# Kernel tuning notes

Measured on AMD Instinct MI355X. Metric: run time of the kernel, lower is better.

## Reference

```python
import jax, jax.numpy as jnp
import numpy as np

HUGE = 1e9  # stand-in for ops.HUGE_INT


def setup_inputs() -> dict:
    key = jax.random.key(0)
    ks = jax.random.split(key, 8)
    B, Q, K = 8, 128, 256
    Dq = Dk = Dv = H = 512
    query = jax.random.normal(ks[0], (B, Q, Dq), dtype=jnp.float32)
    k_ = jax.random.normal(ks[1], (B, K, Dk), dtype=jnp.float32)
    value = jax.random.normal(ks[2], (B, K, Dv), dtype=jnp.float32)
    mask = jax.random.randint(ks[3], (B, K), 0, 2, dtype=jnp.int32)
    # FFN params: linear1 (Dq+Dk -> H, bias), linear2 (H -> 1, no bias)
    W1 = jax.random.normal(ks[4], (Dq + Dk, H), dtype=jnp.float32) * 0.05
    b1 = jax.random.normal(ks[5], (H,), dtype=jnp.float32) * 0.05
    w2 = jax.random.normal(ks[6], (H, 1), dtype=jnp.float32) * 0.05
    return {"query": query, "key": k_, "value": value, "mask": mask,
            "W1": W1, "b1": b1, "w2": w2}


def reference(query, key, value, mask, W1, b1, w2):
    # Additive (FFN) attention. Original tiles query/key into [B, Q*K, Dq+Dk]
    # and applies linear1; concat@W1 is separable, so we project q and k
    # separately and broadcast-add (same math, no tiled concat tensor).
    Dq = query.shape[-1]
    Wq, Wk = W1[:Dq], W1[Dq:]
    q_proj = jnp.einsum('bqd,dh->bqh', query, Wq)   # [B,Q,H]
    k_proj = jnp.einsum('bkd,dh->bkh', key, Wk)     # [B,K,H]
    hidden = jnp.tanh(q_proj[:, :, None, :] + k_proj[:, None, :, :] + b1)  # [B,Q,K,H]
    scores = jnp.einsum('bqkh,h->bqk', hidden, w2[:, 0])  # [B,Q,K]
    # padding mask fill BEFORE scaling, matching the original op order
    scores = jnp.where(mask[:, None, :] != 0, -HUGE, scores)
    scores = scores / jnp.sqrt(jnp.float32(key.shape[-1]))
    attn_weights = jax.nn.softmax(scores, axis=-1)
    attn_vec = jnp.einsum('bqk,bkv->bqv', attn_weights, value)  # dropout=0 at eval
    return attn_vec, attn_weights
```

## Files before the change

### kernel.cpp

```cpp
#include <hip/hip_runtime.h>
#include <hip/hip_bf16.h>

#define B_ 8
#define Q_ 128
#define K_ 256
#define D_ 512
#define TWOLOG2E 2.8853900817779268f
#define SCALE 0.044194173824159216f
#define L2E 1.4426950408889634f
#define MASKVAL (-44194173.824159216f)

typedef __attribute__((ext_vector_type(8))) short frag8;
typedef __attribute__((ext_vector_type(4))) float f32x4;

__device__ __forceinline__ float fexp2(float x) {
  float r;
  asm("v_exp_f32 %0, %1" : "=v"(r) : "v"(x));
  return r;
}
__device__ __forceinline__ float frcp(float x) {
  float r;
  asm("v_rcp_f32 %0, %1" : "=v"(r) : "v"(x));
  return r;
}
__device__ __forceinline__ unsigned f2bf_u(float x) {
  unsigned u = __float_as_uint(x);
  return (u + 0x7FFFu + ((u >> 16) & 1u)) >> 16;
}
__device__ __forceinline__ unsigned short f2bf(float x) {
  return (unsigned short)f2bf_u(x);
}
__device__ __forceinline__ unsigned packbf(float lo, float hi) {
  return f2bf_u(lo) | (f2bf_u(hi) << 16);
}

__global__ __launch_bounds__(256) void gemm_kernel(
    const float* __restrict__ query, const float* __restrict__ key,
    const float* __restrict__ W1, const float* __restrict__ b1,
    float* __restrict__ qp, float* __restrict__ kpbT) {
  __shared__ short As[32 * 64];
  __shared__ short Bs[64 * 64];
  const int t = threadIdx.x;
  const int m0 = blockIdx.y * 32;
  const int n0 = blockIdx.x * 64;
  const bool is_k = (m0 >= B_ * Q_);
  const float* X = is_k ? key : query;
  const int xrow0 = is_k ? (m0 - B_ * Q_) : m0;
  const float* Wb = W1 + (is_k ? (size_t)D_ * D_ : 0);

  const int am = t >> 3;
  const int ac = t & 7;
  const float* gA = X + (size_t)(xrow0 + am) * D_ + ac * 8;
  short* aw = As + am * 64 + ((ac ^ (am & 7)) * 8);

  const int bd = (t & 31) * 2;
  const int bn = t >> 5;
  const float* gB0 = Wb + (size_t)bd * D_ + n0 + bn * 8;
  const float* gB1 = gB0 + D_;
  const int bchunk = bd >> 3;
  const int bsub = bd & 7;

  const int l = t & 63;
  const int w = t >> 6;
  const int lr = l & 15;
  const int kg = l >> 4;
  const int key8 = lr & 7;
  int aoff[2][2], boff[2];
#pragma unroll
  for (int kk = 0; kk < 2; ++kk) {
    const int cpos = ((kg + kk * 4) ^ key8) * 8;
#pragma unroll
    for (int mt = 0; mt < 2; ++mt) aoff[mt][kk] = (mt * 16 + lr) * 64 + cpos;
    boff[kk] = (w * 16 + lr) * 64 + cpos;
  }

  f32x4 acc[2];
  acc[0] = (f32x4){0.f, 0.f, 0.f, 0.f};
  acc[1] = (f32x4){0.f, 0.f, 0.f, 0.f};

  for (int k0 = 0; k0 < D_; k0 += 64) {
    float4 a0 = *(const float4*)(gA + k0);
    float4 a1 = *(const float4*)(gA + k0 + 4);
    const float* p0 = gB0 + (size_t)k0 * D_;
    const float* p1 = gB1 + (size_t)k0 * D_;
    float4 b00 = *(const float4*)(p0);
    float4 b01 = *(const float4*)(p0 + 4);
    float4 b10 = *(const float4*)(p1);
    float4 b11 = *(const float4*)(p1 + 4);
    __syncthreads();
    union { frag8 f; unsigned short u[8]; } av;
    av.u[0] = f2bf(a0.x); av.u[1] = f2bf(a0.y); av.u[2] = f2bf(a0.z); av.u[3] = f2bf(a0.w);
    av.u[4] = f2bf(a1.x); av.u[5] = f2bf(a1.y); av.u[6] = f2bf(a1.z); av.u[7] = f2bf(a1.w);
    *(frag8*)aw = av.f;
    {
      float r0[8] = {b00.x, b00.y, b00.z, b00.w, b01.x, b01.y, b01.z, b01.w};
      float r1[8] = {b10.x, b10.y, b10.z, b10.w, b11.x, b11.y, b11.z, b11.w};
#pragma unroll
      for (int j = 0; j < 8; ++j) {
        const int n = bn * 8 + j;
        const int epos = ((bchunk ^ j) * 8) + bsub;
        *(unsigned*)(Bs + n * 64 + epos) = packbf(r0[j], r1[j]);
      }
    }
    __syncthreads();
#pragma unroll
    for (int kk = 0; kk < 2; ++kk) {
      frag8 bf = *(const frag8*)(Bs + boff[kk]);
#pragma unroll
      for (int mt = 0; mt < 2; ++mt) {
        frag8 af = *(const frag8*)(As + aoff[mt][kk]);
        acc[mt] = __builtin_amdgcn_mfma_f32_16x16x32_bf16(af, bf, acc[mt], 0, 0, 0);
      }
    }
  }

  const int col = n0 + w * 16 + lr;
  if (is_k) {
    const float bc = b1[col];
#pragma unroll
    for (int mt = 0; mt < 2; ++mt) {
      const int krow = m0 - B_ * Q_ + mt * 16 + kg * 4;
      const int bb = krow >> 8;
      const int kk0 = krow & 255;
      float4 v;
      v.x = (acc[mt][0] + bc) * TWOLOG2E;
      v.y = (acc[mt][1] + bc) * TWOLOG2E;
      v.z = (acc[mt][2] + bc) * TWOLOG2E;
      v.w = (acc[mt][3] + bc) * TWOLOG2E;
      *(float4*)&kpbT[((size_t)bb * D_ + col) * K_ + kk0] = v;
    }
  } else {
#pragma unroll
    for (int mt = 0; mt < 2; ++mt) {
#pragma unroll
      for (int i = 0; i < 4; ++i) {
        const int row = m0 + mt * 16 + kg * 4 + i;
        qp[(size_t)row * D_ + col] = acc[mt][i] * TWOLOG2E;
      }
    }
  }
}

__global__ __launch_bounds__(1024) void attn_kernel(
    const float* __restrict__ qp, const float* __restrict__ kpbT,
    const float* __restrict__ value, const int* __restrict__ mask,
    const float* __restrict__ w2,
    float* __restrict__ out_vec, float* __restrict__ out_w) {
  __shared__ float smem_p[16 * 256];
  __shared__ float pw[4 * 256];
  const int b = blockIdx.y;
  const int q0 = blockIdx.x * 4;
  const int t = threadIdx.x;
  const int lane = t & 63;
  const int w = __builtin_amdgcn_readfirstlane(t >> 6);
  const int kc = w & 3;
  const int hq = w >> 2;

  {
    const float* pk = kpbT + ((size_t)b * D_ + hq * 128) * K_ + kc * 64 + lane;
    const float* q_0 = qp + (size_t)(b * Q_ + q0 + 0) * D_ + hq * 128;
    const float* q_1 = qp + (size_t)(b * Q_ + q0 + 1) * D_ + hq * 128;
    const float* q_2 = qp + (size_t)(b * Q_ + q0 + 2) * D_ + hq * 128;
    const float* q_3 = qp + (size_t)(b * Q_ + q0 + 3) * D_ + hq * 128;
    const float* w2h = w2 + hq * 128;

    float a0 = 0.f, a1 = 0.f, a2 = 0.f, a3 = 0.f;
    for (int h = 0; h < 128; h += 8) {
      float kv[8];
#pragma unroll
      for (int j = 0; j < 8; ++j) kv[j] = pk[(size_t)(h + j) * K_];
#pragma unroll
      for (int j = 0; j < 8; ++j) {
        const float wv = w2h[h + j];
        const float r0 = frcp(fexp2(q_0[h + j] + kv[j]) + 1.f);
        const float r1 = frcp(fexp2(q_1[h + j] + kv[j]) + 1.f);
        const float r2 = frcp(fexp2(q_2[h + j] + kv[j]) + 1.f);
        const float r3 = frcp(fexp2(q_3[h + j] + kv[j]) + 1.f);
        a0 = fmaf(wv, r0, a0);
        a1 = fmaf(wv, r1, a1);
        a2 = fmaf(wv, r2, a2);
        a3 = fmaf(wv, r3, a3);
      }
    }
    smem_p[w * 256 + 0 * 64 + lane] = a0;
    smem_p[w * 256 + 1 * 64 + lane] = a1;
    smem_p[w * 256 + 2 * 64 + lane] = a2;
    smem_p[w * 256 + 3 * 64 + lane] = a3;
  }
  __syncthreads();

  if (w < 4) {
    float sw = 0.f;
#pragma unroll
    for (int m = 0; m < 8; ++m) sw += w2[lane + 64 * m];
#pragma unroll
    for (int off = 32; off; off >>= 1) sw += __shfl_xor(sw, off);

    float s[4];
#pragma unroll
    for (int r = 0; r < 4; ++r) {
      float p = smem_p[(0 * 4 + r) * 256 + w * 64 + lane] +
                smem_p[(1 * 4 + r) * 256 + w * 64 + lane] +
                smem_p[(2 * 4 + r) * 256 + w * 64 + lane] +
                smem_p[(3 * 4 + r) * 256 + w * 64 + lane];
      const int mk = mask[b * K_ + r * 64 + lane];
      s[r] = mk ? MASKVAL : fmaf(-2.f, p, sw) * SCALE;
    }
    float mx = fmaxf(fmaxf(s[0], s[1]), fmaxf(s[2], s[3]));
#pragma unroll
    for (int off = 32; off; off >>= 1) mx = fmaxf(mx, __shfl_xor(mx, off));
    float e[4], sum = 0.f;
#pragma unroll
    for (int r = 0; r < 4; ++r) {
      e[r] = fexp2((s[r] - mx) * L2E);
      sum += e[r];
    }
#pragma unroll
    for (int off = 32; off; off >>= 1) sum += __shfl_xor(sum, off);
    const float inv = frcp(sum);
    float* ow = out_w + (size_t)(b * Q_ + q0 + w) * K_;
#pragma unroll
    for (int r = 0; r < 4; ++r) {
      const float p = e[r] * inv;
      pw[w * 256 + r * 64 + lane] = p;
      ow[r * 64 + lane] = p;
    }
  }
  __syncthreads();

  const int col = t & 511;
  const int qq = t >> 9;
  float o0 = 0.f, o1 = 0.f;
  const float* vb = value + (size_t)b * K_ * D_;
  for (int k = 0; k < K_; k += 4) {
    const float4 p0 = *(const float4*)&pw[(qq * 2 + 0) * 256 + k];
    const float4 p1 = *(const float4*)&pw[(qq * 2 + 1) * 256 + k];
    const float v0 = vb[(size_t)(k + 0) * D_ + col];
    const float v1 = vb[(size_t)(k + 1) * D_ + col];
    const float v2 = vb[(size_t)(k + 2) * D_ + col];
    const float v3 = vb[(size_t)(k + 3) * D_ + col];
    o0 = fmaf(p0.x, v0, fmaf(p0.y, v1, fmaf(p0.z, v2, fmaf(p0.w, v3, o0))));
    o1 = fmaf(p1.x, v0, fmaf(p1.y, v1, fmaf(p1.z, v2, fmaf(p1.w, v3, o1))));
  }
  out_vec[(size_t)(b * Q_ + q0 + qq * 2 + 0) * D_ + col] = o0;
  out_vec[(size_t)(b * Q_ + q0 + qq * 2 + 1) * D_ + col] = o1;
}

extern "C" void kernel_launch(void* const* d_in, const int* in_sizes, int n_in,
                              void* d_out, int out_size, void* d_ws, size_t ws_size,
                              hipStream_t stream) {
  const float* query = (const float*)d_in[0];
  const float* key   = (const float*)d_in[1];
  const float* value = (const float*)d_in[2];
  const int*   mask  = (const int*)d_in[3];
  const float* W1    = (const float*)d_in[4];
  const float* b1    = (const float*)d_in[5];
  const float* w2    = (const float*)d_in[6];

  float* out_vec = (float*)d_out;
  float* out_w   = out_vec + (size_t)B_ * Q_ * D_;

  float* qp   = (float*)d_ws;
  float* kpbT = qp + (size_t)B_ * Q_ * D_;

  gemm_kernel<<<dim3(8, 96), 256, 0, stream>>>(query, key, W1, b1, qp, kpbT);
  attn_kernel<<<dim3(Q_ / 4, B_), 1024, 0, stream>>>(qp, kpbT, value, mask, w2,
                                                     out_vec, out_w);
}
```

Measured before the change: 128.0 us.

## Precompute exponentials in projection epilogue and factor exp(q+k) into a product

The GEMM epilogue now stores exp2 of the scaled q and k projections, so the attention inner loop computes exp(q+k) as a product E_q*E_k with one FMA instead of one v_exp per element. This removes the transcendental op from the hot Q*K*H loop, leaving only the reciprocal. Query and w2 values are loaded as float4 vectors. The W1 tile staging is also reorganized into a padded (72-stride) LDS layout with row-pair loads, replacing the XOR swizzle. The risk is overflow or underflow of exp of large projections, which could change the tanh result at extreme values.

After: 113.3 us. -11.5%, faster.

```diff
diff --git a/kernel.cpp b/kernel.cpp
--- a/kernel.cpp
+++ b/kernel.cpp
@@ -39,7 +39,7 @@
     const float* __restrict__ W1, const float* __restrict__ b1,
     float* __restrict__ qp, float* __restrict__ kpbT) {
   __shared__ short As[32 * 64];
-  __shared__ short Bs[64 * 64];
+  __shared__ short Bs[64 * 72];
   const int t = threadIdx.x;
   const int m0 = blockIdx.y * 32;
   const int n0 = blockIdx.x * 64;
@@ -53,12 +53,9 @@
   const float* gA = X + (size_t)(xrow0 + am) * D_ + ac * 8;
   short* aw = As + am * 64 + ((ac ^ (am & 7)) * 8);
 
-  const int bd = (t & 31) * 2;
-  const int bn = t >> 5;
-  const float* gB0 = Wb + (size_t)bd * D_ + n0 + bn * 8;
-  const float* gB1 = gB0 + D_;
-  const int bchunk = bd >> 3;
-  const int bsub = bd & 7;
+  const int prow = t >> 4;
+  const int n4 = (t & 15) * 4;
+  const float* gB = Wb + n0 + n4;
 
   const int l = t & 63;
   const int w = t >> 6;
@@ -68,10 +65,10 @@
   int aoff[2][2], boff[2];
 #pragma unroll
   for (int kk = 0; kk < 2; ++kk) {
-    const int cpos = ((kg + kk * 4) ^ key8) * 8;
-#pragma unroll
-    for (int mt = 0; mt < 2; ++mt) aoff[mt][kk] = (mt * 16 + lr) * 64 + cpos;
-    boff[kk] = (w * 16 + lr) * 64 + cpos;
+    const int cposA = ((kg + kk * 4) ^ key8) * 8;
+#pragma unroll
+    for (int mt = 0; mt < 2; ++mt) aoff[mt][kk] = (mt * 16 + lr) * 64 + cposA;
+    boff[kk] = (w * 16 + lr) * 72 + (kg + kk * 4) * 8;
   }
 
   f32x4 acc[2];
@@ -81,25 +78,26 @@
   for (int k0 = 0; k0 < D_; k0 += 64) {
     float4 a0 = *(const float4*)(gA + k0);
     float4 a1 = *(const float4*)(gA + k0 + 4);
-    const float* p0 = gB0 + (size_t)k0 * D_;
-    const float* p1 = gB1 + (size_t)k0 * D_;
-    float4 b00 = *(const float4*)(p0);
-    float4 b01 = *(const float4*)(p0 + 4);
-    float4 b10 = *(const float4*)(p1);
-    float4 b11 = *(const float4*)(p1 + 4);
+    float4 w00 = *(const float4*)(gB + (size_t)(k0 + 2 * prow) * D_);
+    float4 w01 = *(const float4*)(gB + (size_t)(k0 + 2 * prow + 1) * D_);
+    float4 w10 = *(const float4*)(gB + (size_t)(k0 + 2 * prow + 32) * D_);
+    float4 w11 = *(const float4*)(gB + (size_t)(k0 + 2 * prow + 33) * D_);
     __syncthreads();
-    union { frag8 f; unsigned short u[8]; } av;
-    av.u[0] = f2bf(a0.x); av.u[1] = f2bf(a0.y); av.u[2] = f2bf(a0.z); av.u[3] = f2bf(a0.w);
-    av.u[4] = f2bf(a1.x); av.u[5] = f2bf(a1.y); av.u[6] = f2bf(a1.z); av.u[7] = f2bf(a1.w);
-    *(frag8*)aw = av.f;
     {
-      float r0[8] = {b00.x, b00.y, b00.z, b00.w, b01.x, b01.y, b01.z, b01.w};
-      float r1[8] = {b10.x, b10.y, b10.z, b10.w, b11.x, b11.y, b11.z, b11.w};
-#pragma unroll
-      for (int j = 0; j < 8; ++j) {
-        const int n = bn * 8 + j;
-        const int epos = ((bchunk ^ j) * 8) + bsub;
-        *(unsigned*)(Bs + n * 64 + epos) = packbf(r0[j], r1[j]);
+      union { frag8 f; unsigned short u[8]; } av;
+      av.u[0] = f2bf(a0.x); av.u[1] = f2bf(a0.y); av.u[2] = f2bf(a0.z); av.u[3] = f2bf(a0.w);
+      av.u[4] = f2bf(a1.x); av.u[5] = f2bf(a1.y); av.u[6] = f2bf(a1.z); av.u[7] = f2bf(a1.w);
+      *(frag8*)aw = av.f;
+    }
+    {
+      float lo0[4] = {w00.x, w00.y, w00.z, w00.w};
+      float hi0[4] = {w01.x, w01.y, w01.z, w01.w};
+      float lo1[4] = {w10.x, w10.y, w10.z, w10.w};
+      float hi1[4] = {w11.x, w11.y, w11.z, w11.w};
+#pragma unroll
+      for (int j = 0; j < 4; ++j) {
+        *(unsigned*)(Bs + (n4 + j) * 72 + 2 * prow) = packbf(lo0[j], hi0[j]);
+        *(unsigned*)(Bs + (n4 + j) * 72 + 2 * (prow + 16)) = packbf(lo1[j], hi1[j]);
       }
     }
     __syncthreads();
@@ -123,10 +121,10 @@
       const int bb = krow >> 8;
       const int kk0 = krow & 255;
       float4 v;
-      v.x = (acc[mt][0] + bc) * TWOLOG2E;
-      v.y = (acc[mt][1] + bc) * TWOLOG2E;
-      v.z = (acc[mt][2] + bc) * TWOLOG2E;
-      v.w = (acc[mt][3] + bc) * TWOLOG2E;
+      v.x = fexp2((acc[mt][0] + bc) * TWOLOG2E);
+      v.y = fexp2((acc[mt][1] + bc) * TWOLOG2E);
+      v.z = fexp2((acc[mt][2] + bc) * TWOLOG2E);
+      v.w = fexp2((acc[mt][3] + bc) * TWOLOG2E);
       *(float4*)&kpbT[((size_t)bb * D_ + col) * K_ + kk0] = v;
     }
   } else {
@@ -135,7 +133,7 @@
 #pragma unroll
       for (int i = 0; i < 4; ++i) {
         const int row = m0 + mt * 16 + kg * 4 + i;
-        qp[(size_t)row * D_ + col] = acc[mt][i] * TWOLOG2E;
+        qp[(size_t)row * D_ + col] = fexp2(acc[mt][i] * TWOLOG2E);
       }
     }
   }
@@ -169,17 +167,26 @@
       float kv[8];
 #pragma unroll
       for (int j = 0; j < 8; ++j) kv[j] = pk[(size_t)(h + j) * K_];
+      float4 e0a = *(const float4*)(q_0 + h), e0b = *(const float4*)(q_0 + h + 4);
+      float4 e1a = *(const float4*)(q_1 + h), e1b = *(const float4*)(q_1 + h + 4);
+      float4 e2a = *(const float4*)(q_2 + h), e2b = *(const float4*)(q_2 + h + 4);
+      float4 e3a = *(const float4*)(q_3 + h), e3b = *(const float4*)(q_3 + h + 4);
+      float4 wa = *(const float4*)(w2h + h), wb = *(const float4*)(w2h + h + 4);
+      float E0[8] = {e0a.x, e0a.y, e0a.z, e0a.w, e0b.x, e0b.y, e0b.z, e0b.w};
+      float E1[8] = {e1a.x, e1a.y, e1a.z, e1a.w, e1b.x, e1b.y, e1b.z, e1b.w};
+      float E2[8] = {e2a.x, e2a.y, e2a.z, e2a.w, e2b.x, e2b.y, e2b.z, e2b.w};
+      float E3[8] = {e3a.x, e3a.y, e3a.z, e3a.w, e3b.x, e3b.y, e3b.z, e3b.w};
+      float WV[8] = {wa.x, wa.y, wa.z, wa.w, wb.x, wb.y, wb.z, wb.w};
 #pragma unroll
       for (int j = 0; j < 8; ++j) {
-        const float wv = w2h[h + j];
-        const float r0 = frcp(fexp2(q_0[h + j] + kv[j]) + 1.f);
-        const float r1 = frcp(fexp2(q_1[h + j] + kv[j]) + 1.f);
-        const float r2 = frcp(fexp2(q_2[h + j] + kv[j]) + 1.f);
-        const float r3 = frcp(fexp2(q_3[h + j] + kv[j]) + 1.f);
-        a0 = fmaf(wv, r0, a0);
-        a1 = fmaf(wv, r1, a1);
-        a2 = fmaf(wv, r2, a2);
-        a3 = fmaf(wv, r3, a3);
+        const float r0 = frcp(fmaf(E0[j], kv[j], 1.f));
+        const float r1 = frcp(fmaf(E1[j], kv[j], 1.f));
+        const float r2 = frcp(fmaf(E2[j], kv[j], 1.f));
+        const float r3 = frcp(fmaf(E3[j], kv[j], 1.f));
+        a0 = fmaf(WV[j], r0, a0);
+        a1 = fmaf(WV[j], r1, a1);
+        a2 = fmaf(WV[j], r2, a2);
+        a3 = fmaf(WV[j], r3, a3);
       }
     }
     smem_p[w * 256 + 0 * 64 + lane] = a0;
```
